# Performance work log

Measured on AMD Instinct MI355X. Metric: run time of the kernel, lower is better.

The kernel has to match this reference:

```python
import jax, jax.numpy as jnp
import numpy as np

E = 2      # expansion
G = 8      # groups
K = 128    # num_clusters
N = 1024   # feature_size (dim)
D = E * N // G  # per-group cluster dim = 256
EPS = 1e-12


def _l2norm(v, axis):
    return v / jnp.maximum(jnp.linalg.norm(v, axis=axis, keepdims=True), EPS)


def setup_inputs() -> dict:
    key = jax.random.key(0)
    ks = jax.random.split(key, 8)
    x = jax.random.normal(ks[0], (64, N, 8, 8), dtype=jnp.float32)
    W_inp = jax.random.normal(ks[1], (E * N, N), dtype=jnp.float32) * 0.02
    b_inp = jax.random.uniform(ks[2], (E * N,), dtype=jnp.float32)
    W_g = jax.random.normal(ks[3], (G, E * N), dtype=jnp.float32) * 0.02
    b_g = jax.random.uniform(ks[4], (G,), dtype=jnp.float32)
    W_gk = jax.random.normal(ks[5], (G * K, E * N), dtype=jnp.float32) * 0.02
    b_gk = jax.random.uniform(ks[6], (G * K,), dtype=jnp.float32)
    centroids = jax.random.normal(ks[7], (K, D), dtype=jnp.float32) * 0.1
    return {"x": x, "W_inp": W_inp, "b_inp": b_inp, "W_g": W_g, "b_g": b_g,
            "W_gk": W_gk, "b_gk": b_gk, "centroids": centroids}


def reference(x, W_inp, b_inp, W_g, b_g, W_gk, b_gk, centroids):
    b8, c, h, w = x.shape
    bs = b8 // 8
    # [bs*8, C, H, W] -> [bs, M=8*H*W, N=C]
    x = x.reshape(bs, 8, c, h, w).transpose(0, 2, 1, 3, 4).reshape(bs, c, 8 * h * w)
    x = jnp.transpose(x, (0, 2, 1))            # [bs, M, N]
    M = x.shape[1]
    x = _l2norm(x, axis=2)                     # normalize_input
    x = x @ W_inp.T + b_inp                    # [bs, M, E*N]
    alpha_g = jax.nn.sigmoid(x @ W_g.T + b_g)  # [bs, M, G]
    # NOTE: original uses Softmax(dim=1) -> softmax over token dim M
    alpha_gk = jax.nn.softmax(x @ W_gk.T + b_gk, axis=1)   # [bs, M, G*K]
    alpha_gk = alpha_gk.reshape(bs, M, G, K)
    xr = x.reshape(bs, M, G, D)
    w_full = alpha_g[..., None] * alpha_gk     # [bs, M, G, K]
    # vlad[b,k,d] = sum_{m,g} w*(x - c) = einsum(w,x) - (sum w) * c
    vlad = jnp.einsum('bmgk,bmgd->bkd', w_full, xr) \
        - jnp.sum(w_full, axis=(1, 2))[..., None] * centroids  # [bs, K, D]
    vlad = _l2norm(vlad, axis=-1).reshape(bs, K * D)
    return _l2norm(vlad, axis=1)
```

## Files before the change

kernel.cpp:

```cpp
#include <hip/hip_runtime.h>
#include <hip/hip_bf16.h>
#include <math.h>

#define EPSN 1e-12f
typedef unsigned short ushort_t;

typedef float f32x4 __attribute__((ext_vector_type(4)));
typedef short s16x8 __attribute__((ext_vector_type(8)));
typedef unsigned short u16x8 __attribute__((ext_vector_type(8)));
typedef unsigned short u16x4 __attribute__((ext_vector_type(4)));

__device__ __forceinline__ void gload_lds16(const void* g, void* l) {
  __builtin_amdgcn_global_load_lds((const __attribute__((address_space(1))) void*)g,
                                   (__attribute__((address_space(3))) void*)l, 16, 0, 0);
}

__global__ void k0_ssq(const float* __restrict__ x, float* __restrict__ ssq8) {
  int b8 = blockIdx.x >> 3;
  int cc = blockIdx.x & 7;
  int t = threadIdx.x;
  int s4 = (t & 15) * 4;
  int cg = t >> 4;
  const float* xp = x + (size_t)b8 * 65536 + (size_t)cc * 128 * 64;
  float4 a = {0.f, 0.f, 0.f, 0.f};
#pragma unroll
  for (int j = 0; j < 8; ++j) {
    int c = cg + j * 16;
    float4 v = *(const float4*)(xp + (size_t)c * 64 + s4);
    a.x = fmaf(v.x, v.x, a.x);
    a.y = fmaf(v.y, v.y, a.y);
    a.z = fmaf(v.z, v.z, a.z);
    a.w = fmaf(v.w, v.w, a.w);
  }
  __shared__ float red[16][68];
  *(float4*)&red[cg][s4] = a;
  __syncthreads();
  if (t < 64) {
    float s = 0.f;
#pragma unroll
    for (int g = 0; g < 16; ++g) s += red[g][t];
    ssq8[cc * 4096 + b8 * 64 + t] = s;
  }
}

__global__ void k1_transpose(const float* __restrict__ x, const float* __restrict__ ssq8,
                             __hip_bfloat16* __restrict__ xnb) {
  int ct = blockIdx.x;
  int b8 = blockIdx.y;
  int t = threadIdx.x;
  __shared__ float tile[64][65];
  __shared__ float ivs[64];
  if (t < 64) {
    float s = 0.f;
#pragma unroll
    for (int cc = 0; cc < 8; ++cc) s += ssq8[cc * 4096 + b8 * 64 + t];
    ivs[t] = rsqrtf(fmaxf(s, 1e-24f));
  }
  int s = t & 63, cq = t >> 6;
  const float* xp = x + (size_t)b8 * 65536 + (size_t)ct * 64 * 64;
#pragma unroll
  for (int r = 0; r < 16; ++r) {
    int cl = cq * 16 + r;
    tile[cl][s] = xp[cl * 64 + s];
  }
  __syncthreads();
  int cl = t & 63, sq = t >> 6;
#pragma unroll
  for (int r = 0; r < 16; ++r) {
    int smm = sq * 16 + r;
    int tm = b8 * 64 + smm;
    xnb[(size_t)tm * 1024 + ct * 64 + cl] = __float2bfloat16(tile[cl][smm] * ivs[smm]);
  }
}

__global__ void kpack2(const float* __restrict__ Wi, const float* __restrict__ Wgk,
                       const float* __restrict__ W_g, const float* __restrict__ b_inp,
                       const float* __restrict__ b_g, __hip_bfloat16* __restrict__ oWi,
                       __hip_bfloat16* __restrict__ oWx, ushort_t* __restrict__ oWibT,
                       float* __restrict__ bWg) {
  int bid = blockIdx.x;
  int t = threadIdx.x;
  if (bid < 2048) {
    int i = (bid * 256 + t) * 4;
    float4 v = *(const float4*)(Wi + i);
    oWi[i + 0] = __float2bfloat16(v.x);
    oWi[i + 1] = __float2bfloat16(v.y);
    oWi[i + 2] = __float2bfloat16(v.z);
    oWi[i + 3] = __float2bfloat16(v.w);
  } else if (bid < 4096) {
    int i = ((bid - 2048) * 256 + t) * 4;
    float4 v = *(const float4*)(Wgk + i);
    oWx[i + 0] = __float2bfloat16(v.x);
    oWx[i + 1] = __float2bfloat16(v.y);
    oWx[i + 2] = __float2bfloat16(v.z);
    oWx[i + 3] = __float2bfloat16(v.w);
  } else if (bid < 4112) {
    int i = (bid - 4096) * 1024 + t * 4;
    float4 v = *(const float4*)(W_g + i);
    __hip_bfloat16* o = oWx + 1024 * 2048 + i;
    o[0] = __float2bfloat16(v.x);
    o[1] = __float2bfloat16(v.y);
    o[2] = __float2bfloat16(v.z);
    o[3] = __float2bfloat16(v.w);
  } else if (bid < 4352) {
    int i = (bid - 4112) * 1024 + t * 4;
    ushort_t* o = (ushort_t*)(oWx + 1032 * 2048) + i;
    *(u16x4*)o = (u16x4){0, 0, 0, 0};
  } else if (bid < 4360) {
    int j = bid - 4352;
    const float* row = W_g + (size_t)j * 2048;
    float s = 0.f;
    for (int c = t; c < 2048; c += 256) s = fmaf(b_inp[c], row[c], s);
    __shared__ float red[256];
    red[t] = s;
    __syncthreads();
    for (int o = 128; o > 0; o >>= 1) {
      if (t < o) red[t] += red[t + o];
      __syncthreads();
    }
    if (t == 0) bWg[j] = red[0] + b_g[j];
  } else {
    int tt = bid - 4360;
    int cp0 = (tt >> 4) * 64;
    int c0 = (tt & 15) * 64;
    __shared__ ushort_t tile[64][72];
    int r = t >> 2, cs = (t & 3) * 16;
    const float* src = Wi + (size_t)(cp0 + r) * 1024 + c0 + cs;
#pragma unroll
    for (int j = 0; j < 16; j += 4) {
      float4 v = *(const float4*)(src + j);
      __hip_bfloat16 h0 = __float2bfloat16(v.x), h1 = __float2bfloat16(v.y);
      __hip_bfloat16 h2 = __float2bfloat16(v.z), h3 = __float2bfloat16(v.w);
      tile[r][cs + j + 0] = *(ushort_t*)&h0;
      tile[r][cs + j + 1] = *(ushort_t*)&h1;
      tile[r][cs + j + 2] = *(ushort_t*)&h2;
      tile[r][cs + j + 3] = *(ushort_t*)&h3;
    }
    __syncthreads();
    int c = t >> 2, ms = (t & 3) * 16;
    u16x8 o0, o1;
#pragma unroll
    for (int j = 0; j < 8; ++j) o0[j] = tile[ms + j][c];
#pragma unroll
    for (int j = 0; j < 8; ++j) o1[j] = tile[ms + 8 + j][c];
    ushort_t* dst = oWibT + (size_t)(c0 + c) * 2048 + cp0 + ms;
    *(u16x8*)dst = o0;
    *(u16x8*)(dst + 8) = o1;
  }
}

__launch_bounds__(512, 4)
__global__ void gemm0_splitk(const ushort_t* __restrict__ A, const ushort_t* __restrict__ B,
                             float* __restrict__ Cf) {
  const int Kstride = 2048, N = 1024;
  __shared__ alignas(16) ushort_t SH[32768];
  const int tid = threadIdx.x;
  const int m0 = blockIdx.y * 128, n0 = blockIdx.x * 128;
  const int s = blockIdx.z;
  const int koff = s * 512;
  const int w = tid >> 6, l = tid & 63;
  const int wr = w >> 2, wc = w & 3;
  const int srow = w * 8 + (l >> 3);
  const int ksw = ((l & 7) ^ (l >> 3)) * 8;
  const ushort_t* Ag0 = A + (size_t)(m0 + srow) * Kstride + ksw + koff;
  const ushort_t* Ag1 = A + (size_t)(m0 + 64 + srow) * Kstride + ksw + koff;
  const ushort_t* Bg0 = B + (size_t)(n0 + srow) * Kstride + ksw + koff;
  const ushort_t* Bg1 = B + (size_t)(n0 + 64 + srow) * Kstride + ksw + koff;
  const int l0 = w * 512;
  const int l1 = 4096 + w * 512;

  f32x4 acc[4][2];
#pragma unroll
  for (int i = 0; i < 4; ++i)
#pragma unroll
    for (int j = 0; j < 2; ++j) acc[i][j] = (f32x4){0.f, 0.f, 0.f, 0.f};

  const int sw = l & 7, qq = l >> 4;

#define ASH(buf) (SH + (buf)*8192)
#define BSH(buf) (SH + 16384 + (buf)*8192)
#define STAGE(buf, k0)                               \
  {                                                  \
    gload_lds16(Ag0 + (k0), ASH(buf) + l0);          \
    gload_lds16(Ag1 + (k0), ASH(buf) + l1);          \
    gload_lds16(Bg0 + (k0), BSH(buf) + l0);          \
    gload_lds16(Bg1 + (k0), BSH(buf) + l1);          \
  }
#define COMPUTE(buf)                                                                     \
  {                                                                                      \
    s16x8 af[4][2], bf[2][2];                                                            \
    _Pragma("unroll") for (int kk = 0; kk < 2; ++kk) {                                   \
      int slot = (((kk << 2) + qq) ^ sw) * 8;                                            \
      _Pragma("unroll") for (int mi = 0; mi < 4; ++mi)                                   \
          af[mi][kk] = *(const s16x8*)&ASH(buf)[(wr * 64 + mi * 16 + (l & 15)) * 64 +    \
                                               slot];                                   \
      _Pragma("unroll") for (int ni = 0; ni < 2; ++ni)                                   \
          bf[ni][kk] = *(const s16x8*)&BSH(buf)[(wc * 32 + ni * 16 + (l & 15)) * 64 +    \
                                               slot];                                   \
    }                                                                                    \
    _Pragma("unroll") for (int kk = 0; kk < 2; ++kk)                                     \
        _Pragma("unroll") for (int mi = 0; mi < 4; ++mi)                                 \
            _Pragma("unroll") for (int ni = 0; ni < 2; ++ni)                             \
                acc[mi][ni] = __builtin_amdgcn_mfma_f32_16x16x32_bf16(af[mi][kk],        \
                                                                     bf[ni][kk],        \
                                                                     acc[mi][ni], 0, 0, 0); \
  }

  STAGE(0, 0);
  int buf = 0;
  for (int t = 0; t < 7; ++t) {
    STAGE(buf ^ 1, (t + 1) << 6);
    asm volatile("s_waitcnt vmcnt(4)" ::: "memory");
    __builtin_amdgcn_s_barrier();
    asm volatile("" ::: "memory");
    COMPUTE(buf);
    asm volatile("" ::: "memory");
    __builtin_amdgcn_s_barrier();
    buf ^= 1;
  }
  asm volatile("s_waitcnt vmcnt(0)" ::: "memory");
  __builtin_amdgcn_s_barrier();
  asm volatile("" ::: "memory");
  COMPUTE(buf);
#undef STAGE
#undef COMPUTE
#undef ASH
#undef BSH

  float* Co = Cf + (size_t)s * 1152 * 1024;
#pragma unroll
  for (int mi = 0; mi < 4; ++mi) {
    int row = m0 + wr * 64 + mi * 16 + (l >> 4) * 4;
#pragma unroll
    for (int ni = 0; ni < 2; ++ni) {
      int col = n0 + wc * 32 + ni * 16 + (l & 15);
#pragma unroll
      for (int r = 0; r < 4; ++r)
        Co[(size_t)(row + r) * N + col] = acc[mi][ni][r];
    }
  }
}

__global__ void kpackC(const float* __restrict__ Wc4, ushort_t* __restrict__ dst) {
  int i = (blockIdx.x * 256 + threadIdx.x) * 4;
  float4 a = *(const float4*)(Wc4 + i);
  float4 b = *(const float4*)(Wc4 + 1179648 + i);
  float4 c = *(const float4*)(Wc4 + 2359296 + i);
  float4 d = *(const float4*)(Wc4 + 3538944 + i);
  float4 sv = {a.x + b.x + c.x + d.x, a.y + b.y + c.y + d.y,
               a.z + b.z + c.z + d.z, a.w + b.w + c.w + d.w};
  u16x4 o;
  __hip_bfloat16 h0 = __float2bfloat16(sv.x), h1 = __float2bfloat16(sv.y);
  __hip_bfloat16 h2 = __float2bfloat16(sv.z), h3 = __float2bfloat16(sv.w);
  o[0] = *(ushort_t*)&h0; o[1] = *(ushort_t*)&h1;
  o[2] = *(ushort_t*)&h2; o[3] = *(ushort_t*)&h3;
  *(u16x4*)(dst + i) = o;
}

__launch_bounds__(512, 4)
__global__ void gemm_nt_bf16(const ushort_t* __restrict__ A, const ushort_t* __restrict__ B,
                             ushort_t* __restrict__ C, int K, int N) {
  __shared__ alignas(16) ushort_t SH[32768];
  const int tid = threadIdx.x;
  const int m0 = blockIdx.y * 128, n0 = blockIdx.x * 128;
  const int w = tid >> 6, l = tid & 63;
  const int wr = w >> 2, wc = w & 3;
  const int srow = w * 8 + (l >> 3);
  const int ksw = ((l & 7) ^ (l >> 3)) * 8;
  const ushort_t* Ag0 = A + (size_t)(m0 + srow) * K + ksw;
  const ushort_t* Ag1 = A + (size_t)(m0 + 64 + srow) * K + ksw;
  const ushort_t* Bg0 = B + (size_t)(n0 + srow) * K + ksw;
  const ushort_t* Bg1 = B + (size_t)(n0 + 64 + srow) * K + ksw;
  const int l0 = w * 512;
  const int l1 = 4096 + w * 512;

  f32x4 acc[4][2];
#pragma unroll
  for (int i = 0; i < 4; ++i)
#pragma unroll
    for (int j = 0; j < 2; ++j) acc[i][j] = (f32x4){0.f, 0.f, 0.f, 0.f};

  const int sw = l & 7, qq = l >> 4;

#define ASH(buf) (SH + (buf)*8192)
#define BSH(buf) (SH + 16384 + (buf)*8192)
#define STAGE(buf, k0)                               \
  {                                                  \
    gload_lds16(Ag0 + (k0), ASH(buf) + l0);          \
    gload_lds16(Ag1 + (k0), ASH(buf) + l1);          \
    gload_lds16(Bg0 + (k0), BSH(buf) + l0);          \
    gload_lds16(Bg1 + (k0), BSH(buf) + l1);          \
  }
#define COMPUTE(buf)                                                                     \
  {                                                                                      \
    s16x8 af[4][2], bf[2][2];                                                            \
    _Pragma("unroll") for (int kk = 0; kk < 2; ++kk) {                                   \
      int slot = (((kk << 2) + qq) ^ sw) * 8;                                            \
      _Pragma("unroll") for (int mi = 0; mi < 4; ++mi)                                   \
          af[mi][kk] = *(const s16x8*)&ASH(buf)[(wr * 64 + mi * 16 + (l & 15)) * 64 +    \
                                               slot];                                   \
      _Pragma("unroll") for (int ni = 0; ni < 2; ++ni)                                   \
          bf[ni][kk] = *(const s16x8*)&BSH(buf)[(wc * 32 + ni * 16 + (l & 15)) * 64 +    \
                                               slot];                                   \
    }                                                                                    \
    _Pragma("unroll") for (int kk = 0; kk < 2; ++kk)                                     \
        _Pragma("unroll") for (int mi = 0; mi < 4; ++mi)                                 \
            _Pragma("unroll") for (int ni = 0; ni < 2; ++ni)                             \
                acc[mi][ni] = __builtin_amdgcn_mfma_f32_16x16x32_bf16(af[mi][kk],        \
                                                                     bf[ni][kk],        \
                                                                     acc[mi][ni], 0, 0, 0); \
  }

  const int nt = K >> 6;
  STAGE(0, 0);
  int buf = 0;
  for (int t = 0; t < nt - 1; ++t) {
    STAGE(buf ^ 1, (t + 1) << 6);
    asm volatile("s_waitcnt vmcnt(4)" ::: "memory");
    __builtin_amdgcn_s_barrier();
    asm volatile("" ::: "memory");
    COMPUTE(buf);
    asm volatile("" ::: "memory");
    __builtin_amdgcn_s_barrier();
    buf ^= 1;
  }
  asm volatile("s_waitcnt vmcnt(0)" ::: "memory");
  __builtin_amdgcn_s_barrier();
  asm volatile("" ::: "memory");
  COMPUTE(buf);
#undef STAGE
#undef COMPUTE
#undef ASH
#undef BSH

#pragma unroll
  for (int mi = 0; mi < 4; ++mi) {
    int row = m0 + wr * 64 + mi * 16 + (l >> 4) * 4;
#pragma unroll
    for (int ni = 0; ni < 2; ++ni) {
      int col = n0 + wc * 32 + ni * 16 + (l & 15);
#pragma unroll
      for (int r = 0; r < 4; ++r) {
        __hip_bfloat16 hb = __float2bfloat16(acc[mi][ni][r]);
        C[(size_t)(row + r) * N + col] = *(ushort_t*)&hb;
      }
    }
  }
}

__launch_bounds__(256)
__global__ void k5_softmax(const ushort_t* __restrict__ logitsTb, const float* __restrict__ bWg,
                           float* __restrict__ colsumW, ushort_t* __restrict__ wbT) {
  int wv = (blockIdx.x << 2) + (threadIdx.x >> 6);
  int q = wv >> 3, b = wv & 7;
  int l = threadIdx.x & 63;
  int g = q >> 7;
  size_t base = (size_t)q * 4096 + b * 512 + l * 8;
  u16x8 v8 = *(const u16x8*)(logitsTb + base);
  float vs[8];
#pragma unroll
  for (int i = 0; i < 8; ++i) vs[i] = __uint_as_float(((unsigned)v8[i]) << 16);
  float M = vs[0];
#pragma unroll
  for (int i = 1; i < 8; ++i) M = fmaxf(M, vs[i]);
#pragma unroll
  for (int m = 1; m < 64; m <<= 1) M = fmaxf(M, __shfl_xor(M, m, 64));
  float e[8], S = 0.f;
#pragma unroll
  for (int i = 0; i < 8; ++i) {
    e[i] = expf(vs[i] - M);
    S += e[i];
  }
#pragma unroll
  for (int m = 1; m < 64; m <<= 1) S += __shfl_xor(S, m, 64);
  float R = 1.0f / S;
  u16x8 g8 = *(const u16x8*)(logitsTb + (size_t)(1024 + g) * 4096 + b * 512 + l * 8);
  float bg = bWg[g];
  float wv8[8], wsum = 0.f;
#pragma unroll
  for (int i = 0; i < 8; ++i) {
    float gl = __uint_as_float(((unsigned)g8[i]) << 16);
    float ag = 1.0f / (1.0f + expf(-(gl + bg)));
    wv8[i] = e[i] * R * ag;
    wsum += wv8[i];
  }
#pragma unroll
  for (int m = 1; m < 64; m <<= 1) wsum += __shfl_xor(wsum, m, 64);
  if (l == 0) colsumW[b * 1024 + q] = wsum;
  u16x8 o;
#pragma unroll
  for (int i = 0; i < 8; ++i) {
    __hip_bfloat16 hb = __float2bfloat16(wv8[i]);
    o[i] = *(ushort_t*)&hb;
  }
  *(u16x8*)(wbT + base) = o;
}

__launch_bounds__(256)
__global__ void k6_vlad_mfma(const ushort_t* __restrict__ wbT, const ushort_t* __restrict__ YcT,
                             float* __restrict__ vpart) {
  int kt = blockIdx.x >> 2, dt = blockIdx.x & 3;
  int ms = blockIdx.y, b = blockIdx.z;
  __shared__ alignas(16) ushort_t Ash[2][4096];
  __shared__ alignas(16) ushort_t Bsh[2][4096];
  const int tid = threadIdx.x;
  const int w = tid >> 6, l = tid & 63;
  const int wr = w >> 1, wc = w & 1;
  const int crow = l >> 3;
  const int ksw = ((l & 7) ^ crow) * 8;

  const ushort_t* Ap[2];
  const ushort_t* Bp[2];
  int loff[2];
#pragma unroll
  for (int c = 0; c < 2; ++c) {
    int chunk = w * 2 + c;
    Ap[c] = wbT + (size_t)(kt * 64 + chunk * 8 + crow) * 4096 + b * 512 + ms * 64 + ksw;
    Bp[c] = YcT + (size_t)(dt * 64 + chunk * 8 + crow) * 4096 + b * 512 + ms * 64 + ksw;
    loff[c] = chunk * 512;
  }

  f32x4 acc[2][2];
#pragma unroll
  for (int i = 0; i < 2; ++i)
#pragma unroll
    for (int j = 0; j < 2; ++j) acc[i][j] = (f32x4){0.f, 0.f, 0.f, 0.f};

  const int sw = l & 7, qq = l >> 4;

#define STAGE6(buf, g)                                                       \
  {                                                                          \
    size_t offA = (size_t)(g)*524288;                                        \
    size_t offB = (size_t)(g)*1048576;                                       \
    gload_lds16(Ap[0] + offA, &Ash[buf][loff[0]]);                           \
    gload_lds16(Ap[1] + offA, &Ash[buf][loff[1]]);                           \
    gload_lds16(Bp[0] + offB, &Bsh[buf][loff[0]]);                           \
    gload_lds16(Bp[1] + offB, &Bsh[buf][loff[1]]);                           \
  }
#define COMPUTE6(buf)                                                                    \
  {                                                                                      \
    s16x8 af[2][2], bf[2][2];                                                            \
    _Pragma("unroll") for (int kk = 0; kk < 2; ++kk) {                                   \
      int slot = (((kk << 2) + qq) ^ sw) * 8;                                            \
      _Pragma("unroll") for (int mi = 0; mi < 2; ++mi) {                                 \
        af[mi][kk] = *(const s16x8*)&Ash[buf][(wr * 32 + mi * 16 + (l & 15)) * 64 +      \
                                             slot];                                     \
        bf[mi][kk] = *(const s16x8*)&Bsh[buf][(wc * 32 + mi * 16 + (l & 15)) * 64 +      \
                                             slot];                                     \
      }                                                                                  \
    }                                                                                    \
    _Pragma("unroll") for (int kk = 0; kk < 2; ++kk)                                     \
        _Pragma("unroll") for (int mi = 0; mi < 2; ++mi)                                 \
            _Pragma("unroll") for (int ni = 0; ni < 2; ++ni)                             \
                acc[mi][ni] = __builtin_amdgcn_mfma_f32_16x16x32_bf16(af[mi][kk],        \
                                                                     bf[ni][kk],        \
                                                                     acc[mi][ni], 0, 0, 0); \
  }

  STAGE6(0, 0);
  int buf = 0;
  for (int s = 0; s < 7; ++s) {
    STAGE6(buf ^ 1, s + 1);
    asm volatile("s_waitcnt vmcnt(4)" ::: "memory");
    __builtin_amdgcn_s_barrier();
    asm volatile("" ::: "memory");
    COMPUTE6(buf);
    asm volatile("" ::: "memory");
    __builtin_amdgcn_s_barrier();
    buf ^= 1;
  }
  asm volatile("s_waitcnt vmcnt(0)" ::: "memory");
  __builtin_amdgcn_s_barrier();
  asm volatile("" ::: "memory");
  COMPUTE6(buf);
#undef STAGE6
#undef COMPUTE6

#pragma unroll
  for (int mi = 0; mi < 2; ++mi) {
    int row = kt * 64 + wr * 32 + mi * 16 + (l >> 4) * 4;
#pragma unroll
    for (int ni = 0; ni < 2; ++ni) {
      int col = dt * 64 + wc * 32 + ni * 16 + (l & 15);
#pragma unroll
      for (int r = 0; r < 4; ++r)
        vpart[((size_t)(ms * 8 + b) * 128 + row + r) * 256 + col] = acc[mi][ni][r];
    }
  }
}

__global__ void k7_intranorm(const float* __restrict__ vpart, const float* __restrict__ colsumW,
                             const float* __restrict__ b_inp, const float* __restrict__ cent,
                             float* __restrict__ out, float* __restrict__ ss1) {
  int k = blockIdx.x;
  int b = blockIdx.y;
  int d = threadIdx.x;
  float S = 0.f, bp = 0.f;
#pragma unroll
  for (int g = 0; g < 8; ++g) {
    float cw = colsumW[b * 1024 + g * 128 + k];
    S += cw;
    bp = fmaf(b_inp[g * 256 + d], cw, bp);
  }
  size_t off = ((size_t)b * 128 + k) * 256 + d;
  float v = bp - S * cent[(size_t)k * 256 + d];
#pragma unroll
  for (int i = 0; i < 8; ++i) v += vpart[off + (size_t)i * 262144];
  float ss = v * v;
#pragma unroll
  for (int m = 1; m < 64; m <<= 1) ss += __shfl_xor(ss, m, 64);
  __shared__ float red[4];
  int lane = d & 63, wv = d >> 6;
  if (lane == 0) red[wv] = ss;
  __syncthreads();
  float tot = red[0] + red[1] + red[2] + red[3];
  float rinv = 1.0f / fmaxf(sqrtf(tot), EPSN);
  out[off] = v * rinv;
  if (d == 0) ss1[b * 128 + k] = tot * rinv * rinv;
}

__global__ void k8_finalnorm(const float* __restrict__ ss1, float* __restrict__ out) {
  int b = blockIdx.x;
  int t = threadIdx.x;
  __shared__ float red[256];
  red[t] = (t < 128) ? ss1[b * 128 + t] : 0.f;
  __syncthreads();
  for (int o = 128; o > 0; o >>= 1) {
    if (t < o) red[t] += red[t + o];
    __syncthreads();
  }
  float rinv = 1.0f / fmaxf(sqrtf(red[0]), EPSN);
  float* op = out + (size_t)b * 32768;
  for (int i = t; i < 32768; i += 256) op[i] *= rinv;
}

extern "C" void kernel_launch(void* const* d_in, const int* in_sizes, int n_in,
                              void* d_out, int out_size, void* d_ws, size_t ws_size,
                              hipStream_t stream) {
  const float* x     = (const float*)d_in[0];
  const float* W_inp = (const float*)d_in[1];
  const float* b_inp = (const float*)d_in[2];
  const float* W_g   = (const float*)d_in[3];
  const float* b_g   = (const float*)d_in[4];
  const float* W_gk  = (const float*)d_in[5];
  const float* cent  = (const float*)d_in[7];
  float* out = (float*)d_out;
  float* ws = (float*)d_ws;

  float* ssq8    = ws + 0;
  float* colsumW = ws + 32768;
  float* ss1     = ws + 40960;
  float* bWg     = ws + 41984;
  ushort_t* xnb  = (ushort_t*)(ws + 42048);
  ushort_t* wbT  = xnb;
  ushort_t* stackedA = (ushort_t*)(ws + 2139200);
  ushort_t* WibT = (ushort_t*)(ws + 3777600);
  ushort_t* Wgkx = (ushort_t*)(ws + 4826176);
  float* vpart   = ws + 3777600;
  float* Wc4     = ws + 6005824;
  ushort_t* Cstacked = (ushort_t*)(ws + 6005824);
  ushort_t* YcT      = Cstacked;
  ushort_t* logitsTb = Cstacked + (size_t)2048 * 4096;

  k0_ssq<<<512, 256, 0, stream>>>(x, ssq8);
  k1_transpose<<<dim3(16, 64), 256, 0, stream>>>(x, ssq8, (__hip_bfloat16*)xnb);
  kpack2<<<4872, 256, 0, stream>>>(W_inp, W_gk, W_g, b_inp, b_g,
                                   (__hip_bfloat16*)stackedA, (__hip_bfloat16*)Wgkx, WibT, bWg);
  gemm0_splitk<<<dim3(8, 9, 4), 512, 0, stream>>>(Wgkx, WibT, Wc4);
  kpackC<<<1152, 256, 0, stream>>>(Wc4, stackedA + (size_t)2048 * 1024);
  gemm_nt_bf16<<<dim3(32, 25), 512, 0, stream>>>(stackedA, xnb, Cstacked, 1024, 4096);
  k5_softmax<<<2048, 256, 0, stream>>>(logitsTb, bWg, colsumW, wbT);
  k6_vlad_mfma<<<dim3(8, 8, 8), 256, 0, stream>>>(wbT, YcT, vpart);
  k7_intranorm<<<dim3(128, 8), 256, 0, stream>>>(vpart, colsumW, b_inp, cent, out, ss1);
  k8_finalnorm<<<8, 256, 0, stream>>>(ss1, out);
}
```

Measured before the change: 123.1 us.

## Enlarge main GEMM tile to 256x256 and pad A rows to tile multiple

Replaces the 128x128-tile bf16 GEMM with a 256x256-tile version in which each warp computes 128x64, which doubles data reuse per LDS load. The grid shrinks from 32x25 to 16x13 blocks. The stacked A matrix is padded from 3200 to 3328 rows by an extra zero-fill branch in the pack kernel, and the workspace offsets shift to make room. The cost is more accumulator registers, 128KB of LDS per block and lower occupancy, and 208 blocks may not fill all CUs evenly.

```diff
diff --git a/kernel.cpp b/kernel.cpp
--- a/kernel.cpp
+++ b/kernel.cpp
@@ -119,7 +119,7 @@
       __syncthreads();
     }
     if (t == 0) bWg[j] = red[0] + b_g[j];
-  } else {
+  } else if (bid < 4872) {
     int tt = bid - 4360;
     int cp0 = (tt >> 4) * 64;
     int c0 = (tt & 15) * 64;
@@ -146,6 +146,10 @@
     ushort_t* dst = oWibT + (size_t)(c0 + c) * 2048 + cp0 + ms;
     *(u16x8*)dst = o0;
     *(u16x8*)(dst + 8) = o1;
+  } else {
+    int i = (bid - 4872) * 1024 + t * 4;
+    ushort_t* o = (ushort_t*)oWi + (size_t)3200 * 1024 + i;
+    *(u16x4*)o = (u16x4){0, 0, 0, 0};
   }
 }
 
@@ -257,58 +261,59 @@
   *(u16x4*)(dst + i) = o;
 }
 
-__launch_bounds__(512, 4)
-__global__ void gemm_nt_bf16(const ushort_t* __restrict__ A, const ushort_t* __restrict__ B,
-                             ushort_t* __restrict__ C, int K, int N) {
-  __shared__ alignas(16) ushort_t SH[32768];
+__launch_bounds__(512, 2)
+__global__ void gemm256(const ushort_t* __restrict__ A, const ushort_t* __restrict__ B,
+                        ushort_t* __restrict__ C, int K, int N) {
+  __shared__ alignas(16) ushort_t SH[65536];
   const int tid = threadIdx.x;
-  const int m0 = blockIdx.y * 128, n0 = blockIdx.x * 128;
+  const int m0 = blockIdx.y * 256, n0 = blockIdx.x * 256;
   const int w = tid >> 6, l = tid & 63;
   const int wr = w >> 2, wc = w & 3;
   const int srow = w * 8 + (l >> 3);
   const int ksw = ((l & 7) ^ (l >> 3)) * 8;
-  const ushort_t* Ag0 = A + (size_t)(m0 + srow) * K + ksw;
-  const ushort_t* Ag1 = A + (size_t)(m0 + 64 + srow) * K + ksw;
-  const ushort_t* Bg0 = B + (size_t)(n0 + srow) * K + ksw;
-  const ushort_t* Bg1 = B + (size_t)(n0 + 64 + srow) * K + ksw;
-  const int l0 = w * 512;
-  const int l1 = 4096 + w * 512;
-
-  f32x4 acc[4][2];
-#pragma unroll
-  for (int i = 0; i < 4; ++i)
-#pragma unroll
-    for (int j = 0; j < 2; ++j) acc[i][j] = (f32x4){0.f, 0.f, 0.f, 0.f};
+  const ushort_t* Ag[4];
+  const ushort_t* Bg[4];
+#pragma unroll
+  for (int p = 0; p < 4; ++p) {
+    Ag[p] = A + (size_t)(m0 + p * 64 + srow) * K + ksw;
+    Bg[p] = B + (size_t)(n0 + p * 64 + srow) * K + ksw;
+  }
+  const int ldst = w * 512;
+
+  f32x4 acc[8][4];
+#pragma unroll
+  for (int i = 0; i < 8; ++i)
+#pragma unroll
+    for (int j = 0; j < 4; ++j) acc[i][j] = (f32x4){0.f, 0.f, 0.f, 0.f};
 
   const int sw = l & 7, qq = l >> 4;
 
-#define ASH(buf) (SH + (buf)*8192)
-#define BSH(buf) (SH + 16384 + (buf)*8192)
-#define STAGE(buf, k0)                               \
-  {                                                  \
-    gload_lds16(Ag0 + (k0), ASH(buf) + l0);          \
-    gload_lds16(Ag1 + (k0), ASH(buf) + l1);          \
-    gload_lds16(Bg0 + (k0), BSH(buf) + l0);          \
-    gload_lds16(Bg1 + (k0), BSH(buf) + l1);          \
-  }
-#define COMPUTE(buf)                                                                     \
-  {                                                                                      \
-    s16x8 af[4][2], bf[2][2];                                                            \
-    _Pragma("unroll") for (int kk = 0; kk < 2; ++kk) {                                   \
-      int slot = (((kk << 2) + qq) ^ sw) * 8;                                            \
-      _Pragma("unroll") for (int mi = 0; mi < 4; ++mi)                                   \
-          af[mi][kk] = *(const s16x8*)&ASH(buf)[(wr * 64 + mi * 16 + (l & 15)) * 64 +    \
-                                               slot];                                   \
-      _Pragma("unroll") for (int ni = 0; ni < 2; ++ni)                                   \
-          bf[ni][kk] = *(const s16x8*)&BSH(buf)[(wc * 32 + ni * 16 + (l & 15)) * 64 +    \
-                                               slot];                                   \
-    }                                                                                    \
-    _Pragma("unroll") for (int kk = 0; kk < 2; ++kk)                                     \
-        _Pragma("unroll") for (int mi = 0; mi < 4; ++mi)                                 \
-            _Pragma("unroll") for (int ni = 0; ni < 2; ++ni)                             \
-                acc[mi][ni] = __builtin_amdgcn_mfma_f32_16x16x32_bf16(af[mi][kk],        \
-                                                                     bf[ni][kk],        \
-                                                                     acc[mi][ni], 0, 0, 0); \
+#define ABASE(buf) (SH + (buf)*16384)
+#define BBASE(buf) (SH + 32768 + (buf)*16384)
+#define STAGE(buf, k0)                                           \
+  {                                                              \
+    _Pragma("unroll") for (int p = 0; p < 4; ++p)                \
+        gload_lds16(Ag[p] + (k0), ABASE(buf) + p * 4096 + ldst); \
+    _Pragma("unroll") for (int p = 0; p < 4; ++p)                \
+        gload_lds16(Bg[p] + (k0), BBASE(buf) + p * 4096 + ldst); \
+  }
+
+#define COMPUTE(buf)                                                                      \
+  {                                                                                       \
+    const ushort_t* As = ABASE(buf);                                                      \
+    const ushort_t* Bs = BBASE(buf);                                                      \
+    _Pragma("unroll") for (int kk = 0; kk < 2; ++kk) {                                    \
+      int slot = (((kk << 2) + qq) ^ sw) * 8;                                             \
+      s16x8 bfr[4];                                                                       \
+      _Pragma("unroll") for (int ni = 0; ni < 4; ++ni)                                    \
+          bfr[ni] = *(const s16x8*)&Bs[(wc * 64 + ni * 16 + (l & 15)) * 64 + slot];       \
+      _Pragma("unroll") for (int mi = 0; mi < 8; ++mi) {                                  \
+        s16x8 a = *(const s16x8*)&As[(wr * 128 + mi * 16 + (l & 15)) * 64 + slot];        \
+        _Pragma("unroll") for (int ni = 0; ni < 4; ++ni)                                  \
+            acc[mi][ni] = __builtin_amdgcn_mfma_f32_16x16x32_bf16(a, bfr[ni],             \
+                                                                 acc[mi][ni], 0, 0, 0);  \
+      }                                                                                   \
+    }                                                                                     \
   }
 
   const int nt = K >> 6;
@@ -316,7 +321,7 @@
   int buf = 0;
   for (int t = 0; t < nt - 1; ++t) {
     STAGE(buf ^ 1, (t + 1) << 6);
-    asm volatile("s_waitcnt vmcnt(4)" ::: "memory");
+    asm volatile("s_waitcnt vmcnt(8)" ::: "memory");
     __builtin_amdgcn_s_barrier();
     asm volatile("" ::: "memory");
     COMPUTE(buf);
@@ -330,15 +335,15 @@
   COMPUTE(buf);
 #undef STAGE
 #undef COMPUTE
-#undef ASH
-#undef BSH
-
-#pragma unroll
-  for (int mi = 0; mi < 4; ++mi) {
-    int row = m0 + wr * 64 + mi * 16 + (l >> 4) * 4;
-#pragma unroll
-    for (int ni = 0; ni < 2; ++ni) {
-      int col = n0 + wc * 32 + ni * 16 + (l & 15);
+#undef ABASE
+#undef BBASE
+
+#pragma unroll
+  for (int mi = 0; mi < 8; ++mi) {
+    int row = m0 + wr * 128 + mi * 16 + (l >> 4) * 4;
+#pragma unroll
+    for (int ni = 0; ni < 4; ++ni) {
+      int col = n0 + wc * 64 + ni * 16 + (l & 15);
 #pragma unroll
       for (int r = 0; r < 4; ++r) {
         __hip_bfloat16 hb = __float2bfloat16(acc[mi][ni][r]);
@@ -554,21 +559,21 @@
   ushort_t* xnb  = (ushort_t*)(ws + 42048);
   ushort_t* wbT  = xnb;
   ushort_t* stackedA = (ushort_t*)(ws + 2139200);
-  ushort_t* WibT = (ushort_t*)(ws + 3777600);
-  ushort_t* Wgkx = (ushort_t*)(ws + 4826176);
-  float* vpart   = ws + 3777600;
-  float* Wc4     = ws + 6005824;
-  ushort_t* Cstacked = (ushort_t*)(ws + 6005824);
+  ushort_t* WibT = (ushort_t*)(ws + 3843136);
+  ushort_t* Wgkx = (ushort_t*)(ws + 4891712);
+  float* vpart   = ws + 3843136;
+  float* Wc4     = ws + 6071360;
+  ushort_t* Cstacked = (ushort_t*)(ws + 6071360);
   ushort_t* YcT      = Cstacked;
   ushort_t* logitsTb = Cstacked + (size_t)2048 * 4096;
 
   k0_ssq<<<512, 256, 0, stream>>>(x, ssq8);
   k1_transpose<<<dim3(16, 64), 256, 0, stream>>>(x, ssq8, (__hip_bfloat16*)xnb);
-  kpack2<<<4872, 256, 0, stream>>>(W_inp, W_gk, W_g, b_inp, b_g,
+  kpack2<<<5000, 256, 0, stream>>>(W_inp, W_gk, W_g, b_inp, b_g,
                                    (__hip_bfloat16*)stackedA, (__hip_bfloat16*)Wgkx, WibT, bWg);
   gemm0_splitk<<<dim3(8, 9, 4), 512, 0, stream>>>(Wgkx, WibT, Wc4);
   kpackC<<<1152, 256, 0, stream>>>(Wc4, stackedA + (size_t)2048 * 1024);
-  gemm_nt_bf16<<<dim3(32, 25), 512, 0, stream>>>(stackedA, xnb, Cstacked, 1024, 4096);
+  gemm256<<<dim3(16, 13), 512, 0, stream>>>(stackedA, xnb, Cstacked, 1024, 4096);
   k5_softmax<<<2048, 256, 0, stream>>>(logitsTb, bWg, colsumW, wbT);
   k6_vlad_mfma<<<dim3(8, 8, 8), 256, 0, stream>>>(wbT, YcT, vpart);
   k7_intranorm<<<dim3(128, 8), 256, 0, stream>>>(vpart, colsumW, b_inp, cent, out, ss1);
```

Result: faster. 119.4 us (-3.0%).
